# Optimization experiments

Hardware: AMD Instinct MI355X
Metric: run time of the kernel (lower is better)

Reference implementation:

```python
import jax, jax.numpy as jnp
import numpy as np

H = 1024  # hidden_size


def _cell(x, W, b):
    # x: [S, B, D_in]; W: [4H, D_in]; b: [4H]
    # One big batched matmul over all timesteps (no recurrence exists).
    gates = jnp.einsum('sbd,gd->sbg', x, W) + b  # [S, B, 4H]
    i, f, g, o = jnp.split(gates, 4, axis=-1)
    i = jax.nn.sigmoid(i)
    g = jnp.tanh(g)
    o = jax.nn.sigmoid(o)
    c = i * g
    h = o * jnp.tanh(c)
    return h, c


def setup_inputs() -> dict:
    key = jax.random.key(0)
    ks = jax.random.split(key, 9)
    S, B, D = 2048, 8, 1024
    s = 1.0 / np.sqrt(D)
    s2 = 1.0 / np.sqrt(2 * H)
    return {
        'x': jax.random.normal(ks[0], (S, B, D), dtype=jnp.float32),
        'W_f0': jax.random.uniform(ks[1], (4 * H, D), jnp.float32, -s, s),
        'b_f0': jax.random.uniform(ks[2], (4 * H,), jnp.float32, -s, s),
        'W_b0': jax.random.uniform(ks[3], (4 * H, D), jnp.float32, -s, s),
        'b_b0': jax.random.uniform(ks[4], (4 * H,), jnp.float32, -s, s),
        'W_f1': jax.random.uniform(ks[5], (4 * H, 2 * H), jnp.float32, -s2, s2),
        'b_f1': jax.random.uniform(ks[6], (4 * H,), jnp.float32, -s2, s2),
        'W_b1': jax.random.uniform(ks[7], (4 * H, 2 * H), jnp.float32, -s2, s2),
        'b_b1': jax.random.uniform(ks[8], (4 * H,), jnp.float32, -s2, s2),
    }


def reference(x, W_f0, b_f0, W_b0, b_b0, W_f1, b_f1, W_b1, b_b1):
    out = x
    h_ns, c_ns = [], []
    for (Wf, bf, Wb, bb) in [(W_f0, b_f0, W_b0, b_b0), (W_f1, b_f1, W_b1, b_b1)]:
        h_f, c_f = _cell(out, Wf, bf)  # forward direction
        h_b, c_b = _cell(out, Wb, bb)  # backward direction (same per-t math)
        out = jnp.concatenate([h_f, h_b], axis=-1)  # [S, B, 2H]
        # forward final state is at t = S-1; backward final state at t = 0
        h_ns += [h_f[-1], h_b[0]]
        c_ns += [c_f[-1], c_b[0]]
    h_n = jnp.stack(h_ns, axis=0)  # [num_layers*2, B, H]
    c_n = jnp.stack(c_ns, axis=0)
    return out, h_n, c_n
```

## Files before the change

### kernel.cpp

```cpp
#include <hip/hip_runtime.h>
#include <hip/hip_bf16.h>

#define S_LEN 2048
#define BATCH 8
#define HID   1024
#define NP    3072
#define MROWS 16384

using bf16x8 = __attribute__((ext_vector_type(8))) short;
using f32x16 = __attribute__((ext_vector_type(16))) float;

__device__ __forceinline__ unsigned short f2b(float f) {
  unsigned int u = __builtin_bit_cast(unsigned int, f);
  u += 0x7fffu + ((u >> 16) & 1u);
  return (unsigned short)(u >> 16);
}

__device__ __forceinline__ float sigf(float x) {
  return 1.f / (1.f + __expf(-x));
}
__device__ __forceinline__ float tanh_f(float x) {
  return 2.f / (1.f + __expf(-2.f * x)) - 1.f;
}

__device__ __forceinline__ void load_lds16(const void* g, void* l) {
  __builtin_amdgcn_global_load_lds(
      (const __attribute__((address_space(1))) void*)g,
      (__attribute__((address_space(3))) void*)(unsigned int)(unsigned long long)l,
      16, 0, 0);
}

#define MEMFENCE asm volatile("" ::: "memory")
#define BARRIER  do { MEMFENCE; __builtin_amdgcn_s_barrier(); MEMFENCE; } while (0)

__global__ void cvt_f32_bf16(const float* __restrict__ in,
                             unsigned short* __restrict__ out, int n4) {
  int i = blockIdx.x * blockDim.x + threadIdx.x;
  if (i >= n4) return;
  const float4 v = reinterpret_cast<const float4*>(in)[i];
  ushort4 u;
  u.x = f2b(v.x); u.y = f2b(v.y); u.z = f2b(v.z); u.w = f2b(v.w);
  reinterpret_cast<ushort4*>(out)[i] = u;
}

__global__ void permute_w(const float* __restrict__ W,
                          unsigned short* __restrict__ Wp, int K) {
  long i = ((long)blockIdx.x * blockDim.x + threadIdx.x) * 4;
  int np = (int)(i / K);
  if (np >= NP) return;
  int k0 = (int)(i % K);
  int c32 = np / 96, rem = np % 96;
  int gate = rem >> 5, hl = rem & 31;
  int og = (gate == 0) ? 0 : (gate == 1) ? 2 : 3;
  int n  = og * 1024 + c32 * 32 + hl;
  const float4 v = *reinterpret_cast<const float4*>(W + (long)n * K + k0);
  ushort4 u;
  u.x = f2b(v.x); u.y = f2b(v.y); u.z = f2b(v.z); u.w = f2b(v.w);
  *reinterpret_cast<ushort4*>(Wp + i) = u;
}

__global__ void permute_b(const float* __restrict__ b, float* __restrict__ bp) {
  int np = blockIdx.x * blockDim.x + threadIdx.x;
  if (np >= NP) return;
  int c32 = np / 96, rem = np % 96;
  int gate = rem >> 5, hl = rem & 31;
  int og = (gate == 0) ? 0 : (gate == 1) ? 2 : 3;
  bp[np] = b[og * 1024 + c32 * 32 + hl];
}

#define MFMAOP(a_, b_, c_) \
  c_ = __builtin_amdgcn_mfma_f32_32x32x16_bf16(a_, b_, c_, 0, 0, 0)

template <int MODE>
__global__ void __launch_bounds__(512, 2)
lstm_gemm(const unsigned short* __restrict__ A,
          const unsigned short* __restrict__ WpF,
          const unsigned short* __restrict__ WpB,
          const float* __restrict__ bpF, const float* __restrict__ bpB,
          int K,
          unsigned short* __restrict__ out_bf, float* __restrict__ out_f,
          float* __restrict__ hn, float* __restrict__ cn) {
  __shared__ __align__(16) char lds[122880];

  const int dir = blockIdx.z;
  const unsigned short* __restrict__ Wp = dir ? WpB : WpF;
  const float* __restrict__ bp = dir ? bpB : bpF;
  const int bm = blockIdx.y;
  const int bn = blockIdx.x;

  const int tid  = threadIdx.x;
  const int wid  = tid >> 6;
  const int lane = tid & 63;
  const int wm   = wid >> 2;
  const int wn   = wid & 3;

  const int  nt = K >> 5;
  const long K2 = (long)K * 2;

  const int lls = lane >> 3;
  const int phs = lane & 7;
  const char *s0, *s1, *s2, *s3, *s4;
  int d0, d1, d2, d3, d4;
#define MKSLICE(j, SRC, DD) do {                                   \
    const int sl = wid + 8 * (j);                                  \
    if (sl < 16) {                                    \
      const int line = sl * 8 + lls;                               \
      const int lg   = phs ^ (line & 7);                           \
      const long grow = (long)bm * 256 + line * 2 + (lg >> 2);     \
      SRC = (const char*)A + grow * K2 + (lg & 3) * 16;            \
      DD  = sl * 1024;                                             \
    } else {                                          \
      const int jb = sl - 16;                                      \
      const int line = jb * 8 + lls;                               \
      const int lg   = phs ^ (line & 7);                           \
      const long grow = (long)bn * 384 + line * 2 + (lg >> 2);     \
      SRC = (const char*)Wp + grow * K2 + (lg & 3) * 16;           \
      DD  = 16384 + jb * 1024;                                     \
    }                                                              \
  } while (0)
  MKSLICE(0, s0, d0); MKSLICE(1, s1, d1); MKSLICE(2, s2, d2);
  MKSLICE(3, s3, d3); MKSLICE(4, s4, d4);
#undef MKSLICE

#define ISSUE(T, DB) do {                                          \
    const long ko_ = (long)(T) * 64;                               \
    load_lds16(s0 + ko_, (DB) + d0);                               \
    load_lds16(s1 + ko_, (DB) + d1);                               \
    load_lds16(s2 + ko_, (DB) + d2);                               \
    load_lds16(s3 + ko_, (DB) + d3);                               \
    load_lds16(s4 + ko_, (DB) + d4);                               \
  } while (0)

  const int l31 = lane & 31;
  const int b5  = lane >> 5;
  auto frag_off = [&](int row) {
    const int line = row >> 1;
    const int lg   = (row & 1) * 4 + b5;
    return line * 128 + ((lg ^ (line & 7)) * 16);
  };
  const int a0o = frag_off(wm * 128 + 0  + l31);
  const int a1o = frag_off(wm * 128 + 32 + l31);
  const int a2o = frag_off(wm * 128 + 64 + l31);
  const int a3o = frag_off(wm * 128 + 96 + l31);
  const int b0o = 16384 + frag_off(wn * 96 + 0  + l31);
  const int b1o = 16384 + frag_off(wn * 96 + 32 + l31);
  const int b2o = 16384 + frag_off(wn * 96 + 64 + l31);

  f32x16 acc[4][3];
#pragma unroll
  for (int i = 0; i < 4; ++i)
#pragma unroll
    for (int j = 0; j < 3; ++j)
      acc[i][j] = (f32x16)(0.f);

  char* p0 = lds;
  char* p1 = lds + 40960;
  char* p2 = lds + 81920;

  ISSUE(0, p0); MEMFENCE;
  ISSUE(1, p1); MEMFENCE;
  asm volatile("s_waitcnt vmcnt(5)" ::: "memory");
  BARRIER;

#define KSTEP(X) do {                                              \
    bf16x8 A0 = *(const bf16x8*)(p0 + (a0o ^ (X)));                \
    bf16x8 A1 = *(const bf16x8*)(p0 + (a1o ^ (X)));                \
    bf16x8 A2 = *(const bf16x8*)(p0 + (a2o ^ (X)));                \
    bf16x8 A3 = *(const bf16x8*)(p0 + (a3o ^ (X)));                \
    bf16x8 B0 = *(const bf16x8*)(p0 + (b0o ^ (X)));                \
    bf16x8 B1 = *(const bf16x8*)(p0 + (b1o ^ (X)));                \
    bf16x8 B2 = *(const bf16x8*)(p0 + (b2o ^ (X)));                \
    __builtin_amdgcn_s_setprio(1);                                 \
    MFMAOP(A0, B0, acc[0][0]); MFMAOP(A1, B0, acc[1][0]);          \
    MFMAOP(A2, B0, acc[2][0]); MFMAOP(A3, B0, acc[3][0]);          \
    MFMAOP(A0, B1, acc[0][1]); MFMAOP(A1, B1, acc[1][1]);          \
    MFMAOP(A2, B1, acc[2][1]); MFMAOP(A3, B1, acc[3][1]);          \
    MFMAOP(A0, B2, acc[0][2]); MFMAOP(A1, B2, acc[1][2]);          \
    MFMAOP(A2, B2, acc[2][2]); MFMAOP(A3, B2, acc[3][2]);          \
    __builtin_amdgcn_s_setprio(0);                                 \
  } while (0)

#pragma unroll 1
  for (int t = 0; t < nt; ++t) {
    if (t + 2 < nt) { ISSUE(t + 2, p2); }
    MEMFENCE;
    KSTEP(0);
    KSTEP(32);
    if (t < nt - 2) { asm volatile("s_waitcnt vmcnt(5)" ::: "memory"); }
    else            { asm volatile("s_waitcnt vmcnt(0)" ::: "memory"); }
    BARRIER;
    char* tp = p0; p0 = p1; p1 = p2; p2 = tp;
  }
#undef KSTEP
#undef ISSUE

  const int c32  = bn * 4 + wn;
  const int h    = c32 * 32 + l31;
  const int outcol = dir * HID + h;
  const float bi = bp[c32 * 96 + l31];
  const float bg = bp[c32 * 96 + 32 + l31];
  const float bo = bp[c32 * 96 + 64 + l31];
  const int Lidx = MODE * 2 + dir;
  const int mrow0 = bm * 256 + wm * 128 + b5 * 4;

#pragma unroll
  for (int mf = 0; mf < 4; ++mf) {
#pragma unroll
    for (int r = 0; r < 16; ++r) {
      const int m = mrow0 + mf * 32 + (r & 3) + 8 * (r >> 2);
      const float iv = acc[mf][0][r] + bi;
      const float gv = acc[mf][1][r] + bg;
      const float ov = acc[mf][2][r] + bo;
      const float is = sigf(iv);
      const float gt = tanh_f(gv);
      const float os = sigf(ov);
      const float c  = is * gt;
      const float hv = os * tanh_f(c);
      if (MODE == 0) {
        out_bf[(long)m * 2048 + outcol] = f2b(hv);
      } else {
        out_f[(long)m * 2048 + outcol] = hv;
      }
      const bool wst = (dir == 0) ? (m >= (S_LEN - 1) * BATCH) : (m < BATCH);
      if (wst) {
        const int b = (dir == 0) ? (m - (S_LEN - 1) * BATCH) : m;
        hn[((long)Lidx * BATCH + b) * HID + h] = hv;
        cn[((long)Lidx * BATCH + b) * HID + h] = c;
      }
    }
  }
}

extern "C" void kernel_launch(void* const* d_in, const int* in_sizes, int n_in,
                              void* d_out, int out_size, void* d_ws, size_t ws_size,
                              hipStream_t stream) {
  const float* x    = (const float*)d_in[0];
  const float* W_f0 = (const float*)d_in[1];
  const float* b_f0 = (const float*)d_in[2];
  const float* W_b0 = (const float*)d_in[3];
  const float* b_b0 = (const float*)d_in[4];
  const float* W_f1 = (const float*)d_in[5];
  const float* b_f1 = (const float*)d_in[6];
  const float* W_b1 = (const float*)d_in[7];
  const float* b_b1 = (const float*)d_in[8];

  float* out = (float*)d_out;
  float* hn  = out + (long)MROWS * 2048;
  float* cn  = hn + 4 * BATCH * HID;

  unsigned short* x_bf  = (unsigned short*)d_ws;
  unsigned short* out1  = x_bf + (long)MROWS * 1024;
  unsigned short* wp_f0 = out1 + (long)MROWS * 2048;
  unsigned short* wp_b0 = wp_f0 + (long)NP * 1024;
  unsigned short* wp_f1 = wp_b0 + (long)NP * 1024;
  unsigned short* wp_b1 = wp_f1 + (long)NP * 2048;
  float* bp_f0 = (float*)(wp_b1 + (long)NP * 2048);
  float* bp_b0 = bp_f0 + NP;
  float* bp_f1 = bp_b0 + NP;
  float* bp_b1 = bp_f1 + NP;

  cvt_f32_bf16<<<16384, 256, 0, stream>>>(x, x_bf, MROWS * 1024 / 4);
  permute_w<<<3072, 256, 0, stream>>>(W_f0, wp_f0, 1024);
  permute_w<<<3072, 256, 0, stream>>>(W_b0, wp_b0, 1024);
  permute_w<<<6144, 256, 0, stream>>>(W_f1, wp_f1, 2048);
  permute_w<<<6144, 256, 0, stream>>>(W_b1, wp_b1, 2048);
  permute_b<<<12, 256, 0, stream>>>(b_f0, bp_f0);
  permute_b<<<12, 256, 0, stream>>>(b_b0, bp_b0);
  permute_b<<<12, 256, 0, stream>>>(b_f1, bp_f1);
  permute_b<<<12, 256, 0, stream>>>(b_b1, bp_b1);

  dim3 grid(NP / 384, MROWS / 256, 2);
  lstm_gemm<0><<<grid, 512, 0, stream>>>(x_bf, wp_f0, wp_b0, bp_f0, bp_b0, 1024,
                                         out1, nullptr, hn, cn);
  lstm_gemm<1><<<grid, 512, 0, stream>>>(out1, wp_f1, wp_b1, bp_f1, bp_b1, 2048,
                                         nullptr, out, hn, cn);
}
```

Measured before the change: 739.5 us.

## Prepack weights in MFMA fragment order, fuse prep kernels, switch to double buffering

Weight conversion now writes bf16 weights directly in per-k-tile MFMA fragment order, and A tiles are staged fragment-major. This lets LDS reads use simple contiguous offsets instead of XOR-swizzled addressing. All conversion and permutation kernels are merged into a single prep launch to cut launch overhead. The GEMM mainloop moves from a three-stage to a two-stage LDS pipeline that waits for all loads each iteration. This frees LDS but exposes more load latency.

```diff
diff --git a/kernel.cpp b/kernel.cpp
--- a/kernel.cpp
+++ b/kernel.cpp
@@ -33,39 +33,67 @@
 #define MEMFENCE asm volatile("" ::: "memory")
 #define BARRIER  do { MEMFENCE; __builtin_amdgcn_s_barrier(); MEMFENCE; } while (0)
 
-__global__ void cvt_f32_bf16(const float* __restrict__ in,
-                             unsigned short* __restrict__ out, int n4) {
-  int i = blockIdx.x * blockDim.x + threadIdx.x;
-  if (i >= n4) return;
-  const float4 v = reinterpret_cast<const float4*>(in)[i];
-  ushort4 u;
-  u.x = f2b(v.x); u.y = f2b(v.y); u.z = f2b(v.z); u.w = f2b(v.w);
-  reinterpret_cast<ushort4*>(out)[i] = u;
-}
-
-__global__ void permute_w(const float* __restrict__ W,
-                          unsigned short* __restrict__ Wp, int K) {
-  long i = ((long)blockIdx.x * blockDim.x + threadIdx.x) * 4;
-  int np = (int)(i / K);
-  if (np >= NP) return;
-  int k0 = (int)(i % K);
-  int c32 = np / 96, rem = np % 96;
-  int gate = rem >> 5, hl = rem & 31;
-  int og = (gate == 0) ? 0 : (gate == 1) ? 2 : 3;
-  int n  = og * 1024 + c32 * 32 + hl;
-  const float4 v = *reinterpret_cast<const float4*>(W + (long)n * K + k0);
-  ushort4 u;
-  u.x = f2b(v.x); u.y = f2b(v.y); u.z = f2b(v.z); u.w = f2b(v.w);
-  *reinterpret_cast<ushort4*>(Wp + i) = u;
-}
-
-__global__ void permute_b(const float* __restrict__ b, float* __restrict__ bp) {
-  int np = blockIdx.x * blockDim.x + threadIdx.x;
-  if (np >= NP) return;
-  int c32 = np / 96, rem = np % 96;
-  int gate = rem >> 5, hl = rem & 31;
-  int og = (gate == 0) ? 0 : (gate == 1) ? 2 : 3;
-  bp[np] = b[og * 1024 + c32 * 32 + hl];
+__device__ __forceinline__ void pack_w_dev(const float* __restrict__ W,
+                                           unsigned short* __restrict__ Wp,
+                                           int id, int Kshift, int ntshift) {
+  const int l = id & 63;
+  const int q = id >> 6;
+  const int c = q % 24;
+  const int q24 = q / 24;
+  const int t  = q24 & ((1 << ntshift) - 1);
+  const int bn = q24 >> ntshift;
+  const int nf = c >> 1, ks = c & 1;
+  const int gate = nf % 3, hgrp = nf / 3;
+  const int og = (gate == 0) ? 0 : (gate == 1) ? 2 : 3;
+  const int row = og * 1024 + (bn * 4 + hgrp) * 32 + (l & 31);
+  const int k   = t * 32 + ks * 16 + (l >> 5) * 8;
+  const float* s = W + ((long)row << Kshift) + k;
+  const float4 v0 = *reinterpret_cast<const float4*>(s);
+  const float4 v1 = *reinterpret_cast<const float4*>(s + 4);
+  uint4 o;
+  o.x = (unsigned)f2b(v0.x) | ((unsigned)f2b(v0.y) << 16);
+  o.y = (unsigned)f2b(v0.z) | ((unsigned)f2b(v0.w) << 16);
+  o.z = (unsigned)f2b(v1.x) | ((unsigned)f2b(v1.y) << 16);
+  o.w = (unsigned)f2b(v1.z) | ((unsigned)f2b(v1.w) << 16);
+  *reinterpret_cast<uint4*>(Wp + (long)id * 8) = o;
+}
+
+__global__ void prep(const float* __restrict__ x, unsigned short* __restrict__ x_bf,
+                     const float* __restrict__ Wf0, const float* __restrict__ Wb0,
+                     const float* __restrict__ Wf1, const float* __restrict__ Wb1,
+                     unsigned short* __restrict__ pf0, unsigned short* __restrict__ pb0,
+                     unsigned short* __restrict__ pf1, unsigned short* __restrict__ pb1,
+                     const float* __restrict__ bf0, const float* __restrict__ bb0,
+                     const float* __restrict__ bf1, const float* __restrict__ bb1,
+                     float* __restrict__ bpf0, float* __restrict__ bpb0,
+                     float* __restrict__ bpf1, float* __restrict__ bpb1) {
+  const int blk = blockIdx.x;
+  const int tid = threadIdx.x;
+  if (blk < 16384) {
+    const int i = blk * 256 + tid;
+    const float4 v = reinterpret_cast<const float4*>(x)[i];
+    ushort4 u;
+    u.x = f2b(v.x); u.y = f2b(v.y); u.z = f2b(v.z); u.w = f2b(v.w);
+    reinterpret_cast<ushort4*>(x_bf)[i] = u;
+  } else if (blk < 17920) {
+    pack_w_dev(Wf0, pf0, (blk - 16384) * 256 + tid, 10, 5);
+  } else if (blk < 19456) {
+    pack_w_dev(Wb0, pb0, (blk - 17920) * 256 + tid, 10, 5);
+  } else if (blk < 22528) {
+    pack_w_dev(Wf1, pf1, (blk - 19456) * 256 + tid, 11, 6);
+  } else if (blk < 25600) {
+    pack_w_dev(Wb1, pb1, (blk - 22528) * 256 + tid, 11, 6);
+  } else {
+    const int r = blk - 25600;
+    const int which = r / 12;
+    const int np = (r % 12) * 256 + tid;
+    const float* bs = which == 0 ? bf0 : which == 1 ? bb0 : which == 2 ? bf1 : bb1;
+    float* bd       = which == 0 ? bpf0 : which == 1 ? bpb0 : which == 2 ? bpf1 : bpb1;
+    const int c32 = np / 96, rem = np % 96;
+    const int gate = rem >> 5, hl = rem & 31;
+    const int og = (gate == 0) ? 0 : (gate == 1) ? 2 : 3;
+    bd[np] = bs[og * 1024 + c32 * 32 + hl];
+  }
 }
 
 #define MFMAOP(a_, b_, c_) \
@@ -74,16 +102,16 @@
 template <int MODE>
 __global__ void __launch_bounds__(512, 2)
 lstm_gemm(const unsigned short* __restrict__ A,
-          const unsigned short* __restrict__ WpF,
-          const unsigned short* __restrict__ WpB,
+          const unsigned short* __restrict__ PF,
+          const unsigned short* __restrict__ PB,
           const float* __restrict__ bpF, const float* __restrict__ bpB,
           int K,
           unsigned short* __restrict__ out_bf, float* __restrict__ out_f,
           float* __restrict__ hn, float* __restrict__ cn) {
-  __shared__ __align__(16) char lds[122880];
+  __shared__ __align__(16) char lds[81920];
 
   const int dir = blockIdx.z;
-  const unsigned short* __restrict__ Wp = dir ? WpB : WpF;
+  const unsigned short* __restrict__ Wp = dir ? PB : PF;
   const float* __restrict__ bp = dir ? bpB : bpF;
   const int bm = blockIdx.y;
   const int bn = blockIdx.x;
@@ -93,58 +121,38 @@
   const int lane = tid & 63;
   const int wm   = wid >> 2;
   const int wn   = wid & 3;
+  const int l31  = lane & 31;
+  const int b5   = lane >> 5;
 
   const int  nt = K >> 5;
   const long K2 = (long)K * 2;
 
-  const int lls = lane >> 3;
-  const int phs = lane & 7;
-  const char *s0, *s1, *s2, *s3, *s4;
-  int d0, d1, d2, d3, d4;
-#define MKSLICE(j, SRC, DD) do {                                   \
-    const int sl = wid + 8 * (j);                                  \
-    if (sl < 16) {                                    \
-      const int line = sl * 8 + lls;                               \
-      const int lg   = phs ^ (line & 7);                           \
-      const long grow = (long)bm * 256 + line * 2 + (lg >> 2);     \
-      SRC = (const char*)A + grow * K2 + (lg & 3) * 16;            \
-      DD  = sl * 1024;                                             \
-    } else {                                          \
-      const int jb = sl - 16;                                      \
-      const int line = jb * 8 + lls;                               \
-      const int lg   = phs ^ (line & 7);                           \
-      const long grow = (long)bn * 384 + line * 2 + (lg >> 2);     \
-      SRC = (const char*)Wp + grow * K2 + (lg & 3) * 16;           \
-      DD  = 16384 + jb * 1024;                                     \
-    }                                                              \
+  const char *srcA0, *srcA1;
+  int dA0, dA1;
+  {
+    const int c0 = wid, c1 = wid + 8;
+    srcA0 = (const char*)A + ((long)(bm * 256 + (c0 >> 1) * 32 + l31)) * K2
+            + (c0 & 1) * 32 + b5 * 16;
+    srcA1 = (const char*)A + ((long)(bm * 256 + (c1 >> 1) * 32 + l31)) * K2
+            + (c1 & 1) * 32 + b5 * 16;
+    dA0 = c0 * 1024; dA1 = c1 * 1024;
+  }
+  const char* srcB = (const char*)Wp + (long)bn * nt * 24576 + wid * 1024 + lane * 16;
+  const int dB0 = 16384 + wid * 1024;
+
+#define ISSUE(T) do {                                              \
+    char* d_ = lds + ((T) & 1) * 40960;                            \
+    const long ta_ = (long)(T) * 64;                               \
+    const long tb_ = (long)(T) * 24576;                            \
+    load_lds16(srcA0 + ta_, d_ + dA0);                             \
+    load_lds16(srcA1 + ta_, d_ + dA1);                             \
+    load_lds16(srcB + tb_,         d_ + dB0);                      \
+    load_lds16(srcB + tb_ + 8192,  d_ + dB0 + 8192);               \
+    load_lds16(srcB + tb_ + 16384, d_ + dB0 + 16384);              \
   } while (0)
-  MKSLICE(0, s0, d0); MKSLICE(1, s1, d1); MKSLICE(2, s2, d2);
-  MKSLICE(3, s3, d3); MKSLICE(4, s4, d4);
-#undef MKSLICE
-
-#define ISSUE(T, DB) do {                                          \
-    const long ko_ = (long)(T) * 64;                               \
-    load_lds16(s0 + ko_, (DB) + d0);                               \
-    load_lds16(s1 + ko_, (DB) + d1);                               \
-    load_lds16(s2 + ko_, (DB) + d2);                               \
-    load_lds16(s3 + ko_, (DB) + d3);                               \
-    load_lds16(s4 + ko_, (DB) + d4);                               \
-  } while (0)
-
-  const int l31 = lane & 31;
-  const int b5  = lane >> 5;
-  auto frag_off = [&](int row) {
-    const int line = row >> 1;
-    const int lg   = (row & 1) * 4 + b5;
-    return line * 128 + ((lg ^ (line & 7)) * 16);
-  };
-  const int a0o = frag_off(wm * 128 + 0  + l31);
-  const int a1o = frag_off(wm * 128 + 32 + l31);
-  const int a2o = frag_off(wm * 128 + 64 + l31);
-  const int a3o = frag_off(wm * 128 + 96 + l31);
-  const int b0o = 16384 + frag_off(wn * 96 + 0  + l31);
-  const int b1o = 16384 + frag_off(wn * 96 + 32 + l31);
-  const int b2o = 16384 + frag_off(wn * 96 + 64 + l31);
+
+  const int abase = wm * 8192 + lane * 16;
+  const int bbase = 16384 + wn * 6144 + lane * 16;
 
   f32x16 acc[4][3];
 #pragma unroll
@@ -153,23 +161,14 @@
     for (int j = 0; j < 3; ++j)
       acc[i][j] = (f32x16)(0.f);
 
-  char* p0 = lds;
-  char* p1 = lds + 40960;
-  char* p2 = lds + 81920;
-
-  ISSUE(0, p0); MEMFENCE;
-  ISSUE(1, p1); MEMFENCE;
-  asm volatile("s_waitcnt vmcnt(5)" ::: "memory");
-  BARRIER;
-
-#define KSTEP(X) do {                                              \
-    bf16x8 A0 = *(const bf16x8*)(p0 + (a0o ^ (X)));                \
-    bf16x8 A1 = *(const bf16x8*)(p0 + (a1o ^ (X)));                \
-    bf16x8 A2 = *(const bf16x8*)(p0 + (a2o ^ (X)));                \
-    bf16x8 A3 = *(const bf16x8*)(p0 + (a3o ^ (X)));                \
-    bf16x8 B0 = *(const bf16x8*)(p0 + (b0o ^ (X)));                \
-    bf16x8 B1 = *(const bf16x8*)(p0 + (b1o ^ (X)));                \
-    bf16x8 B2 = *(const bf16x8*)(p0 + (b2o ^ (X)));                \
+#define KSTEP(BUF, S) do {                                         \
+    bf16x8 A0 = *(const bf16x8*)((BUF) + abase +        (S)*1024); \
+    bf16x8 A1 = *(const bf16x8*)((BUF) + abase + 2048 + (S)*1024); \
+    bf16x8 A2 = *(const bf16x8*)((BUF) + abase + 4096 + (S)*1024); \
+    bf16x8 A3 = *(const bf16x8*)((BUF) + abase + 6144 + (S)*1024); \
+    bf16x8 B0 = *(const bf16x8*)((BUF) + bbase +        (S)*1024); \
+    bf16x8 B1 = *(const bf16x8*)((BUF) + bbase + 2048 + (S)*1024); \
+    bf16x8 B2 = *(const bf16x8*)((BUF) + bbase + 4096 + (S)*1024); \
     __builtin_amdgcn_s_setprio(1);                                 \
     MFMAOP(A0, B0, acc[0][0]); MFMAOP(A1, B0, acc[1][0]);          \
     MFMAOP(A2, B0, acc[2][0]); MFMAOP(A3, B0, acc[3][0]);          \
@@ -180,16 +179,18 @@
     __builtin_amdgcn_s_setprio(0);                                 \
   } while (0)
 
+  ISSUE(0);
+  asm volatile("s_waitcnt vmcnt(0)" ::: "memory");
+  BARRIER;
+
 #pragma unroll 1
   for (int t = 0; t < nt; ++t) {
-    if (t + 2 < nt) { ISSUE(t + 2, p2); }
-    MEMFENCE;
-    KSTEP(0);
-    KSTEP(32);
-    if (t < nt - 2) { asm volatile("s_waitcnt vmcnt(5)" ::: "memory"); }
-    else            { asm volatile("s_waitcnt vmcnt(0)" ::: "memory"); }
+    if (t + 1 < nt) { ISSUE(t + 1); }
+    const char* buf = lds + (t & 1) * 40960;
+    KSTEP(buf, 0);
+    KSTEP(buf, 1);
+    asm volatile("s_waitcnt vmcnt(0)" ::: "memory");
     BARRIER;
-    char* tp = p0; p0 = p1; p1 = p2; p2 = tp;
   }
 #undef KSTEP
 #undef ISSUE
@@ -259,15 +260,10 @@
   float* bp_f1 = bp_b0 + NP;
   float* bp_b1 = bp_f1 + NP;
 
-  cvt_f32_bf16<<<16384, 256, 0, stream>>>(x, x_bf, MROWS * 1024 / 4);
-  permute_w<<<3072, 256, 0, stream>>>(W_f0, wp_f0, 1024);
-  permute_w<<<3072, 256, 0, stream>>>(W_b0, wp_b0, 1024);
-  permute_w<<<6144, 256, 0, stream>>>(W_f1, wp_f1, 2048);
-  permute_w<<<6144, 256, 0, stream>>>(W_b1, wp_b1, 2048);
-  permute_b<<<12, 256, 0, stream>>>(b_f0, bp_f0);
-  permute_b<<<12, 256, 0, stream>>>(b_b0, bp_b0);
-  permute_b<<<12, 256, 0, stream>>>(b_f1, bp_f1);
-  permute_b<<<12, 256, 0, stream>>>(b_b1, bp_b1);
+  prep<<<25648, 256, 0, stream>>>(x, x_bf, W_f0, W_b0, W_f1, W_b1,
+                                  wp_f0, wp_b0, wp_f1, wp_b1,
+                                  b_f0, b_b0, b_f1, b_b1,
+                                  bp_f0, bp_b0, bp_f1, bp_b1);
 
   dim3 grid(NP / 384, MROWS / 256, 2);
   lstm_gemm<0><<<grid, 512, 0, stream>>>(x_bf, wp_f0, wp_b0, bp_f0, bp_b0, 1024,
```

Result: faster. 687.8 us (-7.0%).
